# Kernel tuning notes

Measured on AMD Instinct MI355X. Metric: run time of the kernel, lower is better.

## Reference

```python
import jax, jax.numpy as jnp
import numpy as np

N = 30000
IN_DIM = 256
OUT_DIM = 256
H = 4
HEAD_DIM = OUT_DIM // H  # 64
NUM_EDGE_TYPES = 20
NUM_USED_TYPES = 5  # len(EDGE_TYPES); global indices 0..4
E_PER_TYPE = 40000


def setup_inputs() -> dict:
    key = jax.random.key(0)
    ks = jax.random.split(key, 12)
    s = 0.05
    return {
        "h": jax.random.normal(ks[0], (N, IN_DIM), jnp.float32),
        "edge_src": jax.random.randint(ks[1], (NUM_USED_TYPES, E_PER_TYPE), 0, N, jnp.int64 if jax.config.jax_enable_x64 else jnp.int32),
        "edge_tgt": jax.random.randint(ks[2], (NUM_USED_TYPES, E_PER_TYPE), 0, N, jnp.int64 if jax.config.jax_enable_x64 else jnp.int32),
        "kqv_weight": jax.random.normal(ks[3], (3 * OUT_DIM, IN_DIM), jnp.float32) * s,
        "kqv_bias": jax.random.normal(ks[4], (3 * OUT_DIM,), jnp.float32) * s,
        "out_weight": jax.random.normal(ks[5], (OUT_DIM, OUT_DIM), jnp.float32) * s,
        "out_bias": jax.random.normal(ks[6], (OUT_DIM,), jnp.float32) * s,
        "k_rel": jax.random.normal(ks[7], (NUM_EDGE_TYPES, HEAD_DIM, HEAD_DIM), jnp.float32) * s,
        "v_rel": jax.random.normal(ks[8], (NUM_EDGE_TYPES, HEAD_DIM, HEAD_DIM), jnp.float32) * s,
        "skip": jax.random.normal(ks[9], (1,), jnp.float32),
        "p_rel": jax.random.normal(ks[10], (NUM_USED_TYPES, H), jnp.float32),
    }


def reference(h, edge_src, edge_tgt, kqv_weight, kqv_bias, out_weight, out_bias,
              k_rel, v_rel, skip, p_rel):
    n = h.shape[0]
    T, E = edge_src.shape
    d = HEAD_DIM

    # fused KQV projection: [N, 3*D]
    kqv = h @ kqv_weight.T + kqv_bias
    K, Q, V = jnp.split(kqv, 3, axis=-1)
    K = K.reshape(n, H, d)
    Q = Q.reshape(n, H, d)
    V = V.reshape(n, H, d)

    et = jnp.arange(T)  # global edge-type indices 0..T-1
    k_r = k_rel[et]     # [T, d, d]
    v_r = v_rel[et]

    # gather per-edge, per-type; apply relation matmuls
    K_rel = jnp.einsum('tehd,tdf->tehf', K[edge_src], k_r)  # [T,E,H,d]
    V_rel = jnp.einsum('tehd,tdf->tehf', V[edge_src], v_r)
    Q_tgt = Q[edge_tgt]                                     # [T,E,H,d]

    scale = float(d) ** (-0.5)
    alpha = (Q_tgt * K_rel).sum(-1) * scale                 # [T,E,H]
    alpha = alpha * p_rel[et][:, None, :]                   # multiplicative prior

    # flatten all edge types
    TE = T * E
    alpha = alpha.reshape(TE, H)
    V_rel = V_rel.reshape(TE, H, d)
    tgt_all = edge_tgt.reshape(TE)

    # segmented softmax over incoming edges per target node
    amax = jax.ops.segment_max(alpha, tgt_all, num_segments=n)       # [N,H]
    exp_alpha = jnp.exp(alpha - amax[tgt_all])
    exp_sum = jax.ops.segment_sum(exp_alpha, tgt_all, num_segments=n)
    attn = exp_alpha / (exp_sum[tgt_all] + 1e-16)                    # [TE,H]

    msg = attn[..., None] * V_rel                                    # [TE,H,d]
    out = jax.ops.segment_sum(msg, tgt_all, num_segments=n)          # [N,H,d]
    out = out.reshape(n, OUT_DIM)

    out = jax.nn.gelu(out, approximate=False)
    out = out @ out_weight.T + out_bias

    a = jax.nn.sigmoid(skip)  # [1], broadcasts
    return a * out + (1.0 - a) * h
```

## Files before the change

kernel.cpp:

```cpp
#include <hip/hip_runtime.h>
#include <hip/hip_bf16.h>
#include <math.h>

#define N_NODES 30000
#define NHEAD   4
#define HDIM    64
#define NTYPES  5
#define EPT     40000
#define TE      (NTYPES * EPT)
#define KDIM    256
#define NCAT    1792
#define NBLK    118

typedef __attribute__((ext_vector_type(8))) short short8;
typedef __attribute__((ext_vector_type(4))) float f32x4;

__device__ __forceinline__ unsigned short f2bf(float f) {
    __hip_bfloat16 h = __float2bfloat16(f);
    return *reinterpret_cast<unsigned short*>(&h);
}
__device__ __forceinline__ float bf2f(unsigned short u) {
    return __uint_as_float((unsigned)u << 16);
}

__device__ __forceinline__ void gload16(const unsigned short* g, unsigned short* l) {
    __builtin_amdgcn_global_load_lds((const __attribute__((address_space(1))) void*)g,
                                     (__attribute__((address_space(3))) void*)l, 16, 0, 0);
}

__global__ __launch_bounds__(256) void init_kernel(int* __restrict__ deg) {
    const int gid = blockIdx.x * blockDim.x + threadIdx.x;
    if (gid < N_NODES) deg[gid] = 0;
}

__global__ __launch_bounds__(256) void hist_kernel(const int* __restrict__ etgt,
                                                   int* __restrict__ deg) {
    const int stride = gridDim.x * blockDim.x;
    for (int i = blockIdx.x * blockDim.x + threadIdx.x; i < TE; i += stride)
        atomicAdd(&deg[etgt[i]], 1);
}

__global__ __launch_bounds__(256) void scan1_kernel(const int* __restrict__ deg,
                                                    int* __restrict__ bsum) {
    __shared__ int ws[4];
    const int t = threadIdx.x;
    const int gid = blockIdx.x * 256 + t;
    int d = (gid < N_NODES) ? deg[gid] : 0;
    d += __shfl_xor(d, 1);
    d += __shfl_xor(d, 2);
    d += __shfl_xor(d, 4);
    d += __shfl_xor(d, 8);
    d += __shfl_xor(d, 16);
    d += __shfl_xor(d, 32);
    if ((t & 63) == 0) ws[t >> 6] = d;
    __syncthreads();
    if (t == 0) bsum[blockIdx.x] = ws[0] + ws[1] + ws[2] + ws[3];
}

__global__ __launch_bounds__(128) void scan2_kernel(const int* __restrict__ bsum,
                                                    int* __restrict__ boff) {
    __shared__ int s[128];
    const int t = threadIdx.x;
    s[t] = (t < NBLK) ? bsum[t] : 0;
    __syncthreads();
    for (int d = 1; d < 128; d <<= 1) {
        const int v = (t >= d) ? s[t - d] : 0;
        __syncthreads();
        s[t] += v;
        __syncthreads();
    }
    if (t < NBLK) boff[t] = (t > 0) ? s[t - 1] : 0;
}

__global__ __launch_bounds__(256) void scan3_kernel(const int* __restrict__ deg,
                                                    const int* __restrict__ boff,
                                                    int* __restrict__ off,
                                                    int* __restrict__ cursor) {
    __shared__ int s[256];
    const int t = threadIdx.x;
    const int gid = blockIdx.x * 256 + t;
    const int d = (gid < N_NODES) ? deg[gid] : 0;
    s[t] = d;
    __syncthreads();
    for (int dd = 1; dd < 256; dd <<= 1) {
        const int v = (t >= dd) ? s[t - dd] : 0;
        __syncthreads();
        s[t] += v;
        __syncthreads();
    }
    if (gid < N_NODES) {
        const int excl = s[t] - d + boff[blockIdx.x];
        off[gid] = excl;
        cursor[gid] = excl;
    }
}

__global__ __launch_bounds__(256) void scatter_kernel(const int* __restrict__ etgt,
                                                      const int* __restrict__ esrc,
                                                      int* __restrict__ cursor,
                                                      int* __restrict__ perm) {
    const int stride = gridDim.x * blockDim.x;
    for (int e = blockIdx.x * blockDim.x + threadIdx.x; e < TE; e += stride) {
        const int pos = atomicAdd(&cursor[etgt[e]], 1);
        perm[pos] = esrc[e] | ((e / EPT) << 16);
    }
}

__global__ __launch_bounds__(256) void prep_all(const float* __restrict__ kqv_w,
                                                const float* __restrict__ kqv_b,
                                                const float* __restrict__ k_rel,
                                                const float* __restrict__ p_rel,
                                                const float* __restrict__ h,
                                                const float* __restrict__ v_rel,
                                                const float* __restrict__ out_w,
                                                unsigned short* __restrict__ Wcat,
                                                float* __restrict__ bias_cat,
                                                unsigned short* __restrict__ hb,
                                                unsigned short* __restrict__ vrelT,
                                                unsigned short* __restrict__ Wob) {
    const int bid = blockIdx.x;
    const int tid = threadIdx.x;
    if (bid < 1792) {
        const int r = bid, f = tid;
        if (r < 1280) {
            const int t = r >> 8, hh = (r >> 6) & 3, d = r & 63;
            const float sc = 0.125f * p_rel[t * NHEAD + hh];
            float acc = 0.f;
#pragma unroll
            for (int fp = 0; fp < 64; ++fp)
                acc = fmaf(kqv_w[(size_t)(hh * 64 + fp) * 256 + f], k_rel[t * 4096 + fp * 64 + d], acc);
            Wcat[(size_t)r * 256 + f] = f2bf(acc * sc);
            if (f == 0) {
                float b = 0.f;
#pragma unroll
                for (int fp = 0; fp < 64; ++fp)
                    b = fmaf(kqv_b[hh * 64 + fp], k_rel[t * 4096 + fp * 64 + d], b);
                bias_cat[r] = b * sc;
            }
        } else {
            const int src_row = r - 1024;
            Wcat[(size_t)r * 256 + f] = f2bf(kqv_w[(size_t)src_row * 256 + f]);
            if (f == 0) bias_cat[r] = kqv_b[src_row];
        }
    } else if (bid < 9292) {
        const int i = (bid - 1792) * 256 + tid;
        const float4 v = ((const float4*)h)[i];
        ushort4 u;
        u.x = f2bf(v.x); u.y = f2bf(v.y); u.z = f2bf(v.z); u.w = f2bf(v.w);
        ((ushort4*)hb)[i] = u;
    } else if (bid < 9372) {
        const int idx = (bid - 9292) * 256 + tid;
        if (idx < 64 * 320) {
            const int f = idx / 320, k = idx - f * 320;
            vrelT[f * 320 + k] = f2bf(v_rel[(k >> 6) * 4096 + (k & 63) * 64 + f]);
        }
    } else {
        const int i = (bid - 9372) * 256 + tid;
        Wob[i] = f2bf(out_w[i]);
    }
}

__global__ __launch_bounds__(256) void mfma_gemm(const unsigned short* __restrict__ hb,
                                                 const unsigned short* __restrict__ Wcat,
                                                 const float* __restrict__ bias_cat,
                                                 unsigned short* __restrict__ Ccat) {
    __shared__ unsigned short As[2][128 * 32];
    __shared__ unsigned short Bs[2][128 * 32];
    const int orig = blockIdx.x;
    const int xcd = orig & 7, pos = orig >> 3;
    const int q = 3290 / 8, r = 3290 % 8;
    const int wgid = (xcd < r ? xcd * (q + 1) : r * (q + 1) + (xcd - r) * q) + pos;
    const int brow0 = (wgid / 14) * 128;
    const int bcol0 = (wgid % 14) * 128;

    const int t = threadIdx.x;
    const int wid = t >> 6, lane = t & 63;
    const int wr = wid >> 1, wc = wid & 1;
    const int lrow = lane & 15, kb = lane >> 4;
    const int srow = lane >> 2;
    const int schunk = ((lane & 3) ^ ((lane >> 3) & 3)) * 8;
    const int rchunk = (kb ^ ((lrow >> 1) & 3)) * 8;

    const int arow0 = min(brow0 + wid * 16 + srow, N_NODES - 1);
    const int arow1 = min(brow0 + 64 + wid * 16 + srow, N_NODES - 1);
    const int brw0 = bcol0 + wid * 16 + srow;
    const int brw1 = bcol0 + 64 + wid * 16 + srow;

    auto stage = [&](int buf, int kt) {
        gload16(hb + (size_t)arow0 * KDIM + kt + schunk, &As[buf][wid * 512]);
        gload16(hb + (size_t)arow1 * KDIM + kt + schunk, &As[buf][2048 + wid * 512]);
        gload16(Wcat + (size_t)brw0 * KDIM + kt + schunk, &Bs[buf][wid * 512]);
        gload16(Wcat + (size_t)brw1 * KDIM + kt + schunk, &Bs[buf][2048 + wid * 512]);
    };

    f32x4 acc[4][4];
#pragma unroll
    for (int m = 0; m < 4; ++m)
#pragma unroll
        for (int n = 0; n < 4; ++n) acc[m][n] = (f32x4)0.f;

    stage(0, 0);
    __syncthreads();
    int cur = 0;
    for (int kt = 0; kt < KDIM; kt += 32) {
        if (kt + 32 < KDIM) stage(cur ^ 1, kt + 32);
        short8 af[4], bfr[4];
#pragma unroll
        for (int m = 0; m < 4; ++m)
            af[m] = *(const short8*)&As[cur][(wr * 64 + m * 16 + lrow) * 32 + rchunk];
#pragma unroll
        for (int n = 0; n < 4; ++n)
            bfr[n] = *(const short8*)&Bs[cur][(wc * 64 + n * 16 + lrow) * 32 + rchunk];
#pragma unroll
        for (int m = 0; m < 4; ++m)
#pragma unroll
            for (int n = 0; n < 4; ++n)
                acc[m][n] = __builtin_amdgcn_mfma_f32_16x16x32_bf16(af[m], bfr[n], acc[m][n], 0, 0, 0);
        __syncthreads();
        cur ^= 1;
    }

    unsigned short* Ts = &As[0][0];
    float bias4[4];
#pragma unroll
    for (int n = 0; n < 4; ++n) bias4[n] = bias_cat[bcol0 + wc * 64 + n * 16 + lrow];
    const int lrw = wr * 16 + kb * 4;
    const int lcw = wc * 64 + lrow;
#pragma unroll
    for (int m = 0; m < 4; ++m) {
        __syncthreads();
#pragma unroll
        for (int n = 0; n < 4; ++n)
#pragma unroll
            for (int v = 0; v < 4; ++v)
                Ts[(lrw + v) * 132 + lcw + n * 16] = f2bf(acc[m][n][v] + bias4[n]);
        __syncthreads();
#pragma unroll
        for (int rd = 0; rd < 2; ++rd) {
            const int lr = (t >> 4) + rd * 16;
            const int c0 = (t & 15) * 8;
            const int grow = brow0 + (lr >> 4) * 64 + m * 16 + (lr & 15);
            if (grow < N_NODES) {
                const uint2 lo = *(const uint2*)&Ts[lr * 132 + c0];
                const uint2 hi = *(const uint2*)&Ts[lr * 132 + c0 + 4];
                const uint4 o = make_uint4(lo.x, lo.y, hi.x, hi.y);
                *(uint4*)&Ccat[(size_t)grow * NCAT + bcol0 + c0] = o;
            }
        }
    }
}

__global__ __launch_bounds__(256) void edge_fused(const unsigned short* __restrict__ Ccat,
                                                  const int* __restrict__ off,
                                                  const int* __restrict__ perm,
                                                  unsigned short* __restrict__ Acat) {
    const int wid = threadIdx.x >> 6, lane = threadIdx.x & 63;
    const int tgt = (blockIdx.x << 2) + wid;
    const int h = lane >> 4, f0 = (lane & 15) << 2;
    const int off0 = off[tgt];
    const int off1 = (tgt == N_NODES - 1) ? TE : off[tgt + 1];
    const ushort4 qu = *(const ushort4*)(Ccat + (size_t)tgt * NCAT + 1280 + (h << 6) + f0);
    const float qx = bf2f(qu.x), qy = bf2f(qu.y), qz = bf2f(qu.z), qw = bf2f(qu.w);
    const int voff = 1536 + (h << 6) + f0;
    float es = 0.f;
    float4 a0 = make_float4(0, 0, 0, 0), a1 = a0, a2 = a0, a3 = a0, a4 = a0;
    int i = off0;
    while (i < off1) {
        const bool two = (i + 1 < off1);
        const int pk0 = perm[i];
        const int pk1 = two ? perm[i + 1] : pk0;
        const int s0 = pk0 & 0xFFFF, t0 = pk0 >> 16;
        const int s1 = pk1 & 0xFFFF, t1 = pk1 >> 16;
        const size_t rb0 = (size_t)s0 * NCAT, rb1 = (size_t)s1 * NCAT;
        const ushort4 ku0 = *(const ushort4*)(Ccat + rb0 + ((t0 * 4 + h) << 6) + f0);
        const ushort4 vu0 = *(const ushort4*)(Ccat + rb0 + voff);
        const ushort4 ku1 = *(const ushort4*)(Ccat + rb1 + ((t1 * 4 + h) << 6) + f0);
        const ushort4 vu1 = *(const ushort4*)(Ccat + rb1 + voff);
        float p0 = qx * bf2f(ku0.x) + qy * bf2f(ku0.y) + qz * bf2f(ku0.z) + qw * bf2f(ku0.w);
        float p1 = qx * bf2f(ku1.x) + qy * bf2f(ku1.y) + qz * bf2f(ku1.z) + qw * bf2f(ku1.w);
        p0 += __shfl_xor(p0, 1); p1 += __shfl_xor(p1, 1);
        p0 += __shfl_xor(p0, 2); p1 += __shfl_xor(p1, 2);
        p0 += __shfl_xor(p0, 4); p1 += __shfl_xor(p1, 4);
        p0 += __shfl_xor(p0, 8); p1 += __shfl_xor(p1, 8);
        {
            const float ex = __expf(p0);
            es += ex;
            const float mx = ex * bf2f(vu0.x), my = ex * bf2f(vu0.y);
            const float mz = ex * bf2f(vu0.z), mw = ex * bf2f(vu0.w);
            if (t0 == 0)      { a0.x += mx; a0.y += my; a0.z += mz; a0.w += mw; }
            else if (t0 == 1) { a1.x += mx; a1.y += my; a1.z += mz; a1.w += mw; }
            else if (t0 == 2) { a2.x += mx; a2.y += my; a2.z += mz; a2.w += mw; }
            else if (t0 == 3) { a3.x += mx; a3.y += my; a3.z += mz; a3.w += mw; }
            else              { a4.x += mx; a4.y += my; a4.z += mz; a4.w += mw; }
        }
        if (two) {
            const float ex = __expf(p1);
            es += ex;
            const float mx = ex * bf2f(vu1.x), my = ex * bf2f(vu1.y);
            const float mz = ex * bf2f(vu1.z), mw = ex * bf2f(vu1.w);
            if (t1 == 0)      { a0.x += mx; a0.y += my; a0.z += mz; a0.w += mw; }
            else if (t1 == 1) { a1.x += mx; a1.y += my; a1.z += mz; a1.w += mw; }
            else if (t1 == 2) { a2.x += mx; a2.y += my; a2.z += mz; a2.w += mw; }
            else if (t1 == 3) { a3.x += mx; a3.y += my; a3.z += mz; a3.w += mw; }
            else              { a4.x += mx; a4.y += my; a4.z += mz; a4.w += mw; }
        }
        i += two ? 2 : 1;
    }
    const float inv = 1.f / (es + 1e-16f);
    const size_t rr = (size_t)tgt * NHEAD + h;
    unsigned short* base = Acat + rr * (NTYPES * HDIM) + f0;
    ushort4 u;
    u.x = f2bf(a0.x * inv); u.y = f2bf(a0.y * inv); u.z = f2bf(a0.z * inv); u.w = f2bf(a0.w * inv);
    *(ushort4*)(base + 0 * HDIM) = u;
    u.x = f2bf(a1.x * inv); u.y = f2bf(a1.y * inv); u.z = f2bf(a1.z * inv); u.w = f2bf(a1.w * inv);
    *(ushort4*)(base + 1 * HDIM) = u;
    u.x = f2bf(a2.x * inv); u.y = f2bf(a2.y * inv); u.z = f2bf(a2.z * inv); u.w = f2bf(a2.w * inv);
    *(ushort4*)(base + 2 * HDIM) = u;
    u.x = f2bf(a3.x * inv); u.y = f2bf(a3.y * inv); u.z = f2bf(a3.z * inv); u.w = f2bf(a3.w * inv);
    *(ushort4*)(base + 3 * HDIM) = u;
    u.x = f2bf(a4.x * inv); u.y = f2bf(a4.y * inv); u.z = f2bf(a4.z * inv); u.w = f2bf(a4.w * inv);
    *(ushort4*)(base + 4 * HDIM) = u;
}

__global__ __launch_bounds__(256) void tail_fused(const unsigned short* __restrict__ Acat,
                                                  const unsigned short* __restrict__ vrelT,
                                                  const unsigned short* __restrict__ Wob,
                                                  const float* __restrict__ bias,
                                                  float* __restrict__ C,
                                                  const unsigned short* __restrict__ hres,
                                                  const float* __restrict__ skip) {
    __shared__ unsigned short GsAs[64 * 264];
    __shared__ unsigned short Pb[2][256 * 32];
    const int t = threadIdx.x;
    const int wid = t >> 6, lane = t & 63;
    const int lrow = lane & 15, kb = lane >> 4;
    const int n0 = blockIdx.x * 64;
    const size_t ar0 = (size_t)n0 * 4;

    {
        unsigned short* As1 = GsAs;
        unsigned short* Bs1 = &Pb[0][0];
        const int r0 = t >> 2, q0 = (t & 3) * 8;
        f32x4 acc[4][4];
#pragma unroll
        for (int m = 0; m < 4; ++m)
#pragma unroll
            for (int n = 0; n < 4; ++n) acc[m][n] = (f32x4)0.f;

        for (int kt = 0; kt < 320; kt += 32) {
            uint4 a[4];
#pragma unroll
            for (int i = 0; i < 4; ++i) {
                const size_t row = min(ar0 + r0 + 64 * i, (size_t)120000 - 1);
                a[i] = *(const uint4*)(Acat + row * 320 + kt + q0);
            }
            const uint4 b0 = *(const uint4*)(vrelT + (size_t)r0 * 320 + kt + q0);
            __syncthreads();
#pragma unroll
            for (int i = 0; i < 4; ++i)
                *(uint4*)&As1[(r0 + 64 * i) * 40 + q0] = a[i];
            *(uint4*)&Bs1[r0 * 40 + q0] = b0;
            __syncthreads();
            short8 af[4], bf_[4];
#pragma unroll
            for (int m = 0; m < 4; ++m)
                af[m] = *(const short8*)&As1[(wid * 64 + m * 16 + lrow) * 40 + kb * 8];
#pragma unroll
            for (int n = 0; n < 4; ++n)
                bf_[n] = *(const short8*)&Bs1[(n * 16 + lrow) * 40 + kb * 8];
#pragma unroll
            for (int m = 0; m < 4; ++m)
#pragma unroll
                for (int n = 0; n < 4; ++n)
                    acc[m][n] = __builtin_amdgcn_mfma_f32_16x16x32_bf16(af[m], bf_[n], acc[m][n], 0, 0, 0);
            __syncthreads();
        }
#pragma unroll
        for (int m = 0; m < 4; ++m)
#pragma unroll
            for (int v = 0; v < 4; ++v) {
                const int lr = wid * 64 + m * 16 + kb * 4 + v;
#pragma unroll
                for (int n = 0; n < 4; ++n) {
                    const int col = n * 16 + lrow;
                    const float x = acc[m][n][v];
                    const float g = 0.5f * x * (1.f + erff(x * 0.7071067811865475f));
                    GsAs[(lr >> 2) * 264 + (lr & 3) * 64 + col] = f2bf(g);
                }
            }
        __syncthreads();
    }

    {
        const int wc = wid;
        const int srow = lane >> 2;
        const int schunk = ((lane & 3) ^ ((lane >> 3) & 3)) * 8;
        const int rchunk = (kb ^ ((lrow >> 1) & 3)) * 8;
        auto stage2 = [&](int buf, int kt) {
#pragma unroll
            for (int j = 0; j < 4; ++j) {
                const int rowbase = j * 64 + wid * 16;
                gload16(Wob + (size_t)(rowbase + srow) * 256 + kt + schunk,
                        &Pb[buf][rowbase * 32]);
            }
        };
        f32x4 acc[4][4];
#pragma unroll
        for (int m = 0; m < 4; ++m)
#pragma unroll
            for (int n = 0; n < 4; ++n) acc[m][n] = (f32x4)0.f;

        stage2(0, 0);
        __syncthreads();
        int cur = 0;
        for (int kt = 0; kt < 256; kt += 32) {
            if (kt + 32 < 256) stage2(cur ^ 1, kt + 32);
            short8 af[4], bfr[4];
#pragma unroll
            for (int m = 0; m < 4; ++m)
                af[m] = *(const short8*)&GsAs[(m * 16 + lrow) * 264 + kt + kb * 8];
#pragma unroll
            for (int n = 0; n < 4; ++n)
                bfr[n] = *(const short8*)&Pb[cur][(wc * 64 + n * 16 + lrow) * 32 + rchunk];
#pragma unroll
            for (int m = 0; m < 4; ++m)
#pragma unroll
                for (int n = 0; n < 4; ++n)
                    acc[m][n] = __builtin_amdgcn_mfma_f32_16x16x32_bf16(af[m], bfr[n], acc[m][n], 0, 0, 0);
            __syncthreads();
            cur ^= 1;
        }

        const float s = skip[0];
        const float sa = 1.f / (1.f + expf(-s));
        const float sb = 1.f - sa;
        float bias4[4];
#pragma unroll
        for (int n = 0; n < 4; ++n) bias4[n] = bias[wc * 64 + n * 16 + lrow];
#pragma unroll
        for (int m = 0; m < 4; ++m) {
            const int gr0 = n0 + m * 16 + kb * 4;
#pragma unroll
            for (int v = 0; v < 4; ++v) {
                const int grow = gr0 + v;
                if (grow < N_NODES) {
#pragma unroll
                    for (int n = 0; n < 4; ++n) {
                        const int gcol = wc * 64 + n * 16 + lrow;
                        const float val = acc[m][n][v] + bias4[n];
                        C[(size_t)grow * 256 + gcol] = sa * val + sb * bf2f(hres[(size_t)grow * 256 + gcol]);
                    }
                }
            }
        }
    }
}

extern "C" void kernel_launch(void* const* d_in, const int* in_sizes, int n_in,
                              void* d_out, int out_size, void* d_ws, size_t ws_size,
                              hipStream_t stream) {
    const float* h      = (const float*)d_in[0];
    const int*   esrc   = (const int*)d_in[1];
    const int*   etgt   = (const int*)d_in[2];
    const float* kqv_w  = (const float*)d_in[3];
    const float* kqv_b  = (const float*)d_in[4];
    const float* out_w  = (const float*)d_in[5];
    const float* out_b  = (const float*)d_in[6];
    const float* k_rel  = (const float*)d_in[7];
    const float* v_rel  = (const float*)d_in[8];
    const float* skip   = (const float*)d_in[9];
    const float* p_rel  = (const float*)d_in[10];
    float* out = (float*)d_out;

    float* ws = (float*)d_ws;
    unsigned short* Ccat     = (unsigned short*)ws;
    int*            deg      = (int*)(ws + 26880000);
    int*            off      = (int*)(ws + 26910000);
    int*            cursor   = (int*)(ws + 26940000);
    int*            perm     = (int*)(ws + 26970000);
    unsigned short* Acat     = (unsigned short*)(ws + 31010000);
    unsigned short* vrelT    = (unsigned short*)(ws + 50210000);
    unsigned short* Wob      = (unsigned short*)(ws + 50220240);
    unsigned short* hb       = (unsigned short*)(ws + 50253008);
    int*            bsum     = (int*)(ws + 54093008);
    int*            boff     = (int*)(ws + 54093126);
    unsigned short* Wcat     = (unsigned short*)(ws + 45370000);
    float*          bias_cat = ws + 45600000;

    hipLaunchKernelGGL(init_kernel, dim3(NBLK), dim3(256), 0, stream, deg);
    hipLaunchKernelGGL(hist_kernel, dim3(782), dim3(256), 0, stream, etgt, deg);
    hipLaunchKernelGGL(scan1_kernel, dim3(NBLK), dim3(256), 0, stream, deg, bsum);
    hipLaunchKernelGGL(scan2_kernel, dim3(1), dim3(128), 0, stream, bsum, boff);
    hipLaunchKernelGGL(scan3_kernel, dim3(NBLK), dim3(256), 0, stream, deg, boff, off, cursor);
    hipLaunchKernelGGL(scatter_kernel, dim3(782), dim3(256), 0, stream, etgt, esrc, cursor, perm);
    hipLaunchKernelGGL(prep_all, dim3(9628), dim3(256), 0, stream,
                       kqv_w, kqv_b, k_rel, p_rel, h, v_rel, out_w,
                       Wcat, bias_cat, hb, vrelT, Wob);
    hipLaunchKernelGGL(mfma_gemm, dim3(3290), dim3(256), 0, stream,
                       hb, Wcat, bias_cat, Ccat);
    hipLaunchKernelGGL(edge_fused, dim3(N_NODES / 4), dim3(256), 0, stream,
                       Ccat, off, perm, Acat);
    hipLaunchKernelGGL(tail_fused, dim3(469), dim3(256), 0, stream,
                       Acat, vrelT, Wob, out_b, out, hb, skip);
}
```

Baseline: 190.9 us.

## Load MFMA operands directly from global memory in tail kernel, dropping LDS staging

Both GEMM phases of the fused tail kernel now read their MFMA fragments straight from global memory (Acat, vrelT, Wob) instead of staging tiles through shared memory with barriers and double buffering. This removes most __syncthreads and LDS traffic and shrinks the shared-memory footprint, which can raise occupancy. In exchange, each wave issues redundant, less-coalesced global loads (16-byte strided rows) and relies on L1/L2 caching for reuse of vrelT and Wob.

```diff
diff --git a/kernel.cpp b/kernel.cpp
--- a/kernel.cpp
+++ b/kernel.cpp
@@ -329,8 +329,7 @@
                                                   float* __restrict__ C,
                                                   const unsigned short* __restrict__ hres,
                                                   const float* __restrict__ skip) {
-    __shared__ unsigned short GsAs[64 * 264];
-    __shared__ unsigned short Pb[2][256 * 32];
+    __shared__ unsigned short Gs[64 * 264];
     const int t = threadIdx.x;
     const int wid = t >> 6, lane = t & 63;
     const int lrow = lane & 15, kb = lane >> 4;
@@ -338,42 +337,30 @@
     const size_t ar0 = (size_t)n0 * 4;
 
     {
-        unsigned short* As1 = GsAs;
-        unsigned short* Bs1 = &Pb[0][0];
-        const int r0 = t >> 2, q0 = (t & 3) * 8;
         f32x4 acc[4][4];
 #pragma unroll
         for (int m = 0; m < 4; ++m)
 #pragma unroll
             for (int n = 0; n < 4; ++n) acc[m][n] = (f32x4)0.f;
 
+        size_t arow[4];
+#pragma unroll
+        for (int m = 0; m < 4; ++m)
+            arow[m] = min(ar0 + (size_t)(wid * 64 + m * 16 + lrow), (size_t)120000 - 1);
+
         for (int kt = 0; kt < 320; kt += 32) {
-            uint4 a[4];
-#pragma unroll
-            for (int i = 0; i < 4; ++i) {
-                const size_t row = min(ar0 + r0 + 64 * i, (size_t)120000 - 1);
-                a[i] = *(const uint4*)(Acat + row * 320 + kt + q0);
-            }
-            const uint4 b0 = *(const uint4*)(vrelT + (size_t)r0 * 320 + kt + q0);
-            __syncthreads();
-#pragma unroll
-            for (int i = 0; i < 4; ++i)
-                *(uint4*)&As1[(r0 + 64 * i) * 40 + q0] = a[i];
-            *(uint4*)&Bs1[r0 * 40 + q0] = b0;
-            __syncthreads();
             short8 af[4], bf_[4];
 #pragma unroll
             for (int m = 0; m < 4; ++m)
-                af[m] = *(const short8*)&As1[(wid * 64 + m * 16 + lrow) * 40 + kb * 8];
+                af[m] = *(const short8*)(Acat + arow[m] * 320 + kt + kb * 8);
 #pragma unroll
             for (int n = 0; n < 4; ++n)
-                bf_[n] = *(const short8*)&Bs1[(n * 16 + lrow) * 40 + kb * 8];
+                bf_[n] = *(const short8*)(vrelT + (size_t)(n * 16 + lrow) * 320 + kt + kb * 8);
 #pragma unroll
             for (int m = 0; m < 4; ++m)
 #pragma unroll
                 for (int n = 0; n < 4; ++n)
                     acc[m][n] = __builtin_amdgcn_mfma_f32_16x16x32_bf16(af[m], bf_[n], acc[m][n], 0, 0, 0);
-            __syncthreads();
         }
 #pragma unroll
         for (int m = 0; m < 4; ++m)
@@ -385,50 +372,33 @@
                     const int col = n * 16 + lrow;
                     const float x = acc[m][n][v];
                     const float g = 0.5f * x * (1.f + erff(x * 0.7071067811865475f));
-                    GsAs[(lr >> 2) * 264 + (lr & 3) * 64 + col] = f2bf(g);
+                    Gs[(lr >> 2) * 264 + (lr & 3) * 64 + col] = f2bf(g);
                 }
             }
-        __syncthreads();
-    }
+    }
+    __syncthreads();
 
     {
         const int wc = wid;
-        const int srow = lane >> 2;
-        const int schunk = ((lane & 3) ^ ((lane >> 3) & 3)) * 8;
-        const int rchunk = (kb ^ ((lrow >> 1) & 3)) * 8;
-        auto stage2 = [&](int buf, int kt) {
-#pragma unroll
-            for (int j = 0; j < 4; ++j) {
-                const int rowbase = j * 64 + wid * 16;
-                gload16(Wob + (size_t)(rowbase + srow) * 256 + kt + schunk,
-                        &Pb[buf][rowbase * 32]);
-            }
-        };
         f32x4 acc[4][4];
 #pragma unroll
         for (int m = 0; m < 4; ++m)
 #pragma unroll
             for (int n = 0; n < 4; ++n) acc[m][n] = (f32x4)0.f;
 
-        stage2(0, 0);
-        __syncthreads();
-        int cur = 0;
         for (int kt = 0; kt < 256; kt += 32) {
-            if (kt + 32 < 256) stage2(cur ^ 1, kt + 32);
             short8 af[4], bfr[4];
 #pragma unroll
             for (int m = 0; m < 4; ++m)
-                af[m] = *(const short8*)&GsAs[(m * 16 + lrow) * 264 + kt + kb * 8];
+                af[m] = *(const short8*)&Gs[(m * 16 + lrow) * 264 + kt + kb * 8];
 #pragma unroll
             for (int n = 0; n < 4; ++n)
-                bfr[n] = *(const short8*)&Pb[cur][(wc * 64 + n * 16 + lrow) * 32 + rchunk];
+                bfr[n] = *(const short8*)(Wob + (size_t)(wc * 64 + n * 16 + lrow) * 256 + kt + kb * 8);
 #pragma unroll
             for (int m = 0; m < 4; ++m)
 #pragma unroll
                 for (int n = 0; n < 4; ++n)
                     acc[m][n] = __builtin_amdgcn_mfma_f32_16x16x32_bf16(af[m], bfr[n], acc[m][n], 0, 0, 0);
-            __syncthreads();
-            cur ^= 1;
         }
 
         const float s = skip[0];
```

Result: faster. 178.1 us, median of 2 (-6.7%).
